# Optimization experiments

Hardware: AMD Instinct MI355X
Metric: run time of the kernel (lower is better)

The kernel has to match this reference:

```python
import jax, jax.numpy as jnp
import numpy as np

# norse default LIFParameters
DT = 1e-3
TAU_SYN_INV = 200.0
TAU_MEM_INV = 100.0
V_LEAK = 0.0
V_TH = 1.0
V_RESET = 0.0


def heaviside(x):
    return (x > 0).astype(x.dtype)


def setup_inputs() -> dict:
    key = jax.random.key(0)
    ks = jax.random.split(key, 5)
    T, B, I, H, O = 14, 4096, 2048, 1024, 128
    x = (jax.random.uniform(ks[0], (T, B, I), dtype=jnp.float32) < 0.2).astype(jnp.float32)  # spike train
    w_in = jax.random.normal(ks[1], (H, I), dtype=jnp.float32) * (1.0 / np.sqrt(I))
    w_rec = jax.random.normal(ks[2], (H, H), dtype=jnp.float32) * (1.0 / np.sqrt(H))
    out_w = jax.random.normal(ks[3], (O, H), dtype=jnp.float32) * (1.0 / np.sqrt(H))
    out_b = jax.random.normal(ks[4], (O,), dtype=jnp.float32) * 0.01
    return {"x": x, "w_in": w_in, "w_rec": w_rec, "out_w": out_w, "out_b": out_b}


def reference(x, w_in, w_rec, out_w, out_b):
    T, B, _ = x.shape
    H = w_in.shape[0]
    z0 = jnp.zeros((B, H), dtype=x.dtype)
    v0 = jnp.full((B, H), V_LEAK, dtype=x.dtype)
    i0 = jnp.zeros((B, H), dtype=x.dtype)

    def step(carry, x_t):
        z, v, i = carry
        v_dec = v + DT * TAU_MEM_INV * ((V_LEAK - v) + i)   # membrane integration
        i_dec = i - DT * TAU_SYN_INV * i                    # synaptic decay
        z_new = heaviside(v_dec - V_TH)                     # spike
        v_new = (1.0 - z_new) * v_dec + z_new * V_RESET     # reset
        i_new = i_dec + x_t @ w_in.T + z @ w_rec.T          # input + recurrent current
        return (z_new, v_new, i_new), None

    (z_T, _, _), _ = jax.lax.scan(step, (z0, v0, i0), x)
    return z_T @ out_w.T + out_b
```

## Files before the change

### kernel.cpp

```cpp
#include <hip/hip_runtime.h>
#include <stdint.h>

#define T_STEPS 14
#define B_DIM   4096
#define I_DIM   2048
#define H_DIM   1024
#define O_DIM   128
#define K_TOT   3072
#define ZBYTES  ((size_t)B_DIM * H_DIM)

#define WSCALE_F 33554432.0f

typedef __bf16  bf16x8  __attribute__((ext_vector_type(8)));
typedef float   floatx4 __attribute__((ext_vector_type(4)));
typedef int     int4v   __attribute__((ext_vector_type(4)));
typedef int     int16v  __attribute__((ext_vector_type(16)));
typedef unsigned long long u64;

__device__ __forceinline__ uint16_t f2bf_rne(float f) {
    uint32_t u = __float_as_uint(f);
    u += 0x7fffu + ((u >> 16) & 1u);
    return (uint16_t)(u >> 16);
}
__device__ __forceinline__ float bf2f(uint16_t h) {
    return __uint_as_float(((uint32_t)h) << 16);
}

__device__ __forceinline__ void gload_lds16(const void* g, void* l) {
    __builtin_amdgcn_global_load_lds((__attribute__((address_space(1))) void*)g,
                                     (__attribute__((address_space(3))) void*)l, 16, 0, 0);
}


__global__ void split_w_kernel(const float* __restrict__ w_in, const float* __restrict__ w_rec,
                               int8_t* __restrict__ WB) {
    int idx = blockIdx.x * 256 + threadIdx.x;
    int h = idx / K_TOT;
    int k = idx - h * K_TOT;
    float w = (k < I_DIM) ? w_in[(size_t)h * I_DIM + k]
                          : w_rec[(size_t)h * H_DIM + (k - I_DIM)];
    int W  = __float2int_rn(w * WSCALE_F);
    int d0 = (int8_t)(W & 0xFF);
    int r1 = (W - d0) >> 8;
    int d1 = (int8_t)(r1 & 0xFF);
    int d2 = (r1 - d1) >> 8;
    int nt = h >> 5, n32 = h & 31;
    int ktw = k >> 7, k128 = k & 127;
    int kk = k128 >> 5, half = (k128 >> 4) & 1, j = k128 & 15;
    int lane = half * 32 + n32;
    size_t base = (size_t)(nt * 24 + ktw) * 12288 + kk * 1024 + lane * 16 + j;
    WB[base] = (int8_t)d0; WB[base + 4096] = (int8_t)d1; WB[base + 8192] = (int8_t)d2;
}

__global__ void split_ow_kernel(const float* __restrict__ out_w, uint16_t* __restrict__ OW3) {
    int idx = blockIdx.x * 256 + threadIdx.x;
    float w = out_w[idx];
    uint16_t hi = f2bf_rne(w);
    float r1 = w - bf2f(hi);
    uint16_t mid = f2bf_rne(r1);
    float r2 = r1 - bf2f(mid);
    uint16_t lo = f2bf_rne(r2);
    const size_t S = (size_t)O_DIM * H_DIM;
    OW3[idx] = hi; OW3[idx + S] = mid; OW3[idx + 2 * S] = lo;
}

__global__ void cvt_x_kernel(const float* __restrict__ x, int8_t* __restrict__ xb) {
    size_t gid = (size_t)blockIdx.x * 256 + threadIdx.x;
    int g = (int)(gid & 1023);
    size_t chunk = gid >> 10;
    int kt   = (int)(chunk & 15);
    int mIdx = (int)((chunk >> 4) & 31);
    int t    = (int)(chunk >> 9);
    int group = g >> 8, kk = (g >> 6) & 3, lane = g & 63;
    int half = lane >> 5, row32 = lane & 31;
    int b = mIdx * 128 + group * 32 + row32;
    int k = kt * 128 + kk * 32 + half * 16;
    const float4* src = (const float4*)(x + ((size_t)t * B_DIM + b) * I_DIM + k);
    union { int8_t bytes[16]; int4v v; } u;
#pragma unroll
    for (int q = 0; q < 4; ++q) {
        float4 f = src[q];
        u.bytes[q * 4 + 0] = (int8_t)(f.x > 0.5f);
        u.bytes[q * 4 + 1] = (int8_t)(f.y > 0.5f);
        u.bytes[q * 4 + 2] = (int8_t)(f.z > 0.5f);
        u.bytes[q * 4 + 3] = (int8_t)(f.w > 0.5f);
    }
    ((int4v*)xb)[gid] = u.v;
}

__global__ void zero_cnt_kernel(uint32_t* __restrict__ cnt) {
    __hip_atomic_store(&cnt[blockIdx.x * 256 + threadIdx.x], 0u,
                       __ATOMIC_RELAXED, __HIP_MEMORY_SCOPE_AGENT);
}

__device__ __forceinline__ void loadA(const int8_t* __restrict__ aP, int4v (&a)[4]) {
    a[0] = *(const int4v*)(aP);
    a[1] = *(const int4v*)(aP + 1024);
    a[2] = *(const int4v*)(aP + 2048);
    a[3] = *(const int4v*)(aP + 3072);
}

__device__ __forceinline__ void stage_b0(const int8_t* __restrict__ bChunk0,
                                         int8_t* sB0, int wave, int lane) {
    gload_lds16(bChunk0 + (size_t)wave * 1024 + lane * 16,       sB0 + wave * 1024);
    gload_lds16(bChunk0 + (size_t)(4 + wave) * 1024 + lane * 16, sB0 + (4 + wave) * 1024);
    gload_lds16(bChunk0 + (size_t)(8 + wave) * 1024 + lane * 16, sB0 + (8 + wave) * 1024);
}

__device__ __forceinline__ void lif_iter(const int8_t* __restrict__ aPn,
                                         const int8_t* __restrict__ bPn,
                                         const int8_t* cur, int8_t* nxt,
                                         int4v (&aA)[4],
                                         int wave, int lane, bool stage_next,
                                         int16v (&acc)[3]) {
    if (stage_next) {
        gload_lds16(bPn + (size_t)wave * 1024 + lane * 16,       nxt + wave * 1024);
        gload_lds16(bPn + (size_t)(4 + wave) * 1024 + lane * 16, nxt + (4 + wave) * 1024);
        gload_lds16(bPn + (size_t)(8 + wave) * 1024 + lane * 16, nxt + (8 + wave) * 1024);
        __builtin_amdgcn_sched_barrier(0);
        asm volatile("s_waitcnt vmcnt(3)" ::: "memory");
    } else {
        asm volatile("s_waitcnt vmcnt(0)" ::: "memory");
    }
    __builtin_amdgcn_s_barrier();
    __builtin_amdgcn_sched_barrier(0);
    __builtin_amdgcn_s_setprio(1);
#pragma unroll
    for (int kk = 0; kk < 4; ++kk) {
#pragma unroll
        for (int s = 0; s < 3; ++s) {
            int4v bF = *(const int4v*)(cur + s * 4096 + kk * 1024 + lane * 16);
            acc[s] = __builtin_amdgcn_mfma_i32_32x32x32_i8(aA[kk], bF, acc[s], 0, 0, 0);
        }
    }
    __builtin_amdgcn_s_setprio(0);
    __builtin_amdgcn_sched_barrier(0);
    if (aPn) loadA(aPn, aA);
    asm volatile("s_waitcnt lgkmcnt(0)" ::: "memory");
    __builtin_amdgcn_s_barrier();
}

template<int NKT>
__device__ __forceinline__ void run_phase(const int8_t* __restrict__ aW,
                                          const int8_t* __restrict__ bC,
                                          int8_t* sB0, int8_t* sB1,
                                          int4v (&aA)[4],
                                          int wave, int lane, int16v (&acc)[3]) {
#pragma unroll 1
    for (int kt = 0; kt + 2 < NKT; kt += 2) {
        lif_iter(aW + (size_t)(kt + 1) * 16384, bC + (size_t)(kt + 1) * 12288,
                 sB0, sB1, aA, wave, lane, true, acc);
        lif_iter(aW + (size_t)(kt + 2) * 16384, bC + (size_t)(kt + 2) * 12288,
                 sB1, sB0, aA, wave, lane, true, acc);
    }
    lif_iter(aW + (size_t)(NKT - 1) * 16384, bC + (size_t)(NKT - 1) * 12288,
             sB0, sB1, aA, wave, lane, true, acc);
    lif_iter(nullptr, nullptr, sB1, sB0, aA, wave, lane, false, acc);
}

__launch_bounds__(256, 4)
__global__ void lif_persist_kernel(const int8_t* __restrict__ Xall,
                                   const int8_t* __restrict__ WB,
                                   int8_t* __restrict__ ZS,
                                   uint16_t* __restrict__ Zbf,
                                   uint32_t* __restrict__ cnt) {
    __shared__ int8_t sB0[12288];
    __shared__ int8_t sB1[12288];
    __shared__ int8_t sZ[4096];

    const int tid  = threadIdx.x;
    const int wave = tid >> 6, lane = tid & 63;
    const int lane32 = lane & 31, hl = lane >> 5;

    const int bid = blockIdx.x;
    const int xs = bid & 7, q = bid >> 3;
    const int mIdx = xs * 4 + (q & 3);
    const int nt   = q >> 2;

    const int mBase = mIdx * 128, nBase = nt * 32;
    const int8_t* wbStrip = WB + (size_t)nt * 24 * 12288;
    const int fragOff = wave * 4096 + lane * 16;

    float vmem[16], isyn[16];
#pragma unroll
    for (int r = 0; r < 16; ++r) { vmem[r] = 0.0f; isyn[r] = 0.0f; }

    int4v aA[4];

    stage_b0(wbStrip, sB0, wave, lane);
    loadA(Xall + (size_t)mIdx * 16 * 16384 + fragOff, aA);

    for (int t = 0; t < T_STEPS; ++t) {
        int16v acc[3] = {};

        const int8_t* XtW = Xall + (size_t)t * ((size_t)B_DIM * I_DIM)
                          + (size_t)mIdx * 16 * 16384 + fragOff;
        run_phase<16>(XtW, wbStrip, sB0, sB1, aA, wave, lane, acc);

        if (t > 0) {
            const int8_t* zbChunk = wbStrip + (size_t)16 * 12288;
            stage_b0(zbChunk, sB0, wave, lane);
            if (tid == 0) {
                const uint32_t* f = cnt + ((size_t)mIdx * 13 + (t - 1)) * 32;
                while (__hip_atomic_load((uint32_t*)f, __ATOMIC_RELAXED, __HIP_MEMORY_SCOPE_AGENT) < 32u)
                    __builtin_amdgcn_s_sleep(2);
            }
            __syncthreads();
            const int8_t* zW = ZS + (size_t)(t - 1) * ZBYTES + (size_t)mIdx * 8 * 16384 + fragOff;
            loadA(zW, aA);
            run_phase<8>(zW, zbChunk, sB0, sB1, aA, wave, lane, acc);
        }

        if (t + 1 < T_STEPS) {
            stage_b0(wbStrip, sB0, wave, lane);
            loadA(Xall + (size_t)(t + 1) * ((size_t)B_DIM * I_DIM)
                  + (size_t)mIdx * 16 * 16384 + fragOff, aA);
        }

#pragma unroll
        for (int r = 0; r < 16; ++r) {
#pragma clang fp contract(off)
            float cur = (float)acc[2][r] * (1.0f / 512.0f)
                      + (float)acc[1][r] * (1.0f / 131072.0f)
                      + (float)acc[0][r] * (1.0f / 33554432.0f);
            int row = (r & 3) + 8 * (r >> 2) + 4 * hl;
            float v_dec = vmem[r] + 0.1f * ((0.0f - vmem[r]) + isyn[r]);
            float i_dec = isyn[r] - 0.2f * isyn[r];
            bool z = (v_dec > 1.0f);
            vmem[r] = z ? 0.0f : v_dec;
            isyn[r] = i_dec + cur;
            if (t == T_STEPS - 1) {
                int b = mBase + wave * 32 + row;
                int h = nBase + lane32;
                Zbf[(size_t)b * H_DIM + h] = z ? (uint16_t)0x3F80 : (uint16_t)0;
            } else {
                sZ[wave * 1024 + ((lane32 >> 4) * 32 + row) * 16 + (lane32 & 15)]
                    = z ? (int8_t)1 : (int8_t)0;
            }
        }

        if (t < T_STEPS - 1) {
            __syncthreads();
            const u64* sp = (const u64*)&sZ[tid * 16];
            u64 v0 = sp[0], v1 = sp[1];
            int8_t* dst = ZS + (size_t)t * ZBYTES + ((size_t)mIdx * 8 + (nt >> 2)) * 16384
                        + (tid >> 6) * 4096 + (nt & 3) * 1024 + (tid & 63) * 16;
            __hip_atomic_store((u64*)dst,       v0, __ATOMIC_RELAXED, __HIP_MEMORY_SCOPE_AGENT);
            __hip_atomic_store((u64*)(dst + 8), v1, __ATOMIC_RELAXED, __HIP_MEMORY_SCOPE_AGENT);
            __syncthreads();
            if (tid == 0)
                __hip_atomic_fetch_add(&cnt[((size_t)mIdx * 13 + t) * 32], 1u,
                                       __ATOMIC_RELAXED, __HIP_MEMORY_SCOPE_AGENT);
        }
    }
}

__launch_bounds__(256)
__global__ void out_gemm_kernel(const uint16_t* __restrict__ Zfin,
                                const uint16_t* __restrict__ OW3,
                                const float* __restrict__ out_b,
                                float* __restrict__ out) {
    __shared__ uint16_t sA[16 * 32];
    __shared__ uint16_t sB[3][128 * 32];

    const int tid  = threadIdx.x;
    const int wave = tid >> 6, lane = tid & 63;
    const int quad = lane >> 4, col = lane & 15;

    const int mBase = blockIdx.x * 16;

    floatx4 acc[2] = {};

    const int ldRow = lane >> 2;
    const int ldCol = (lane & 3) * 8;

    for (int kt = 0; kt < H_DIM / 32; ++kt) {
        const int kb = kt * 32;
        __syncthreads();
        if (wave == 0) {
            const uint16_t* g = Zfin + (size_t)(mBase + ldRow) * H_DIM + kb + ldCol;
            gload_lds16(g, &sA[0]);
        }
#pragma unroll
        for (int s = 0; s < 3; ++s) {
            const uint16_t* wsrc = OW3 + (size_t)s * O_DIM * H_DIM;
#pragma unroll
            for (int j = 0; j < 2; ++j) {
                const int rseg = j * 4 + wave;
                const uint16_t* g = wsrc + (size_t)(rseg * 16 + ldRow) * H_DIM + kb + ldCol;
                gload_lds16(g, &sB[s][rseg * 16 * 32]);
            }
        }
        __syncthreads();

        bf16x8 aF = *reinterpret_cast<const bf16x8*>(&sA[col * 32 + quad * 8]);
#pragma unroll
        for (int s = 0; s < 3; ++s) {
#pragma unroll
            for (int ni = 0; ni < 2; ++ni) {
                int row = wave * 32 + ni * 16 + col;
                bf16x8 bF = *reinterpret_cast<const bf16x8*>(&sB[s][row * 32 + quad * 8]);
                acc[ni] = __builtin_amdgcn_mfma_f32_16x16x32_bf16(aF, bF, acc[ni], 0, 0, 0);
            }
        }
    }

    {
#pragma clang fp contract(off)
#pragma unroll
        for (int ni = 0; ni < 2; ++ni)
#pragma unroll
            for (int r = 0; r < 4; ++r) {
                int b = mBase + quad * 4 + r;
                int h = wave * 32 + ni * 16 + col;
                out[(size_t)b * O_DIM + h] = acc[ni][r] + out_b[h];
            }
    }
}

extern "C" void kernel_launch(void* const* d_in, const int* in_sizes, int n_in,
                              void* d_out, int out_size, void* d_ws, size_t ws_size,
                              hipStream_t stream) {
    const float* x     = (const float*)d_in[0];
    const float* w_in  = (const float*)d_in[1];
    const float* w_rec = (const float*)d_in[2];
    const float* out_w = (const float*)d_in[3];
    const float* out_b = (const float*)d_in[4];
    float* out = (float*)d_out;

    char* ws = (char*)d_ws;
    size_t off = 0;
    int8_t*   WB   = (int8_t*)(ws + off);   off += (size_t)3 * H_DIM * K_TOT;
    uint16_t* OW3  = (uint16_t*)(ws + off); off += (size_t)3 * O_DIM * H_DIM * 2;
    int8_t*   Xall = (int8_t*)(ws + off);   off += (size_t)T_STEPS * B_DIM * I_DIM;
    uint16_t* Zbf  = (uint16_t*)(ws + off); off += (size_t)B_DIM * H_DIM * 2;
    int8_t*   ZS   = (int8_t*)(ws + off);   off += (size_t)13 * ZBYTES;
    uint32_t* CNT  = (uint32_t*)(ws + off); off += (size_t)32 * 13 * 32 * 4;

    split_w_kernel<<<(H_DIM * K_TOT) / 256, 256, 0, stream>>>(w_in, w_rec, WB);
    split_ow_kernel<<<(O_DIM * H_DIM) / 256, 256, 0, stream>>>(out_w, OW3);
    cvt_x_kernel<<<(int)(((size_t)T_STEPS * B_DIM * I_DIM / 16) / 256), 256, 0, stream>>>(x, Xall);
    zero_cnt_kernel<<<(32 * 13 * 32) / 256, 256, 0, stream>>>(CNT);

    lif_persist_kernel<<<dim3(1024), dim3(256), 0, stream>>>(Xall, WB, ZS, Zbf, CNT);

    out_gemm_kernel<<<B_DIM / 16, 256, 0, stream>>>(Zbf, OW3, out_b, out);
}
```

Before: 1.295 ms.

## Widen persistent LIF tile to 64 hidden columns per block, halving grid

Each persistent block now computes two 32-column N tiles (64 hidden units) instead of one. It stages both weight strips into doubled LDS buffers and reuses each loaded A fragment (spikes) across six MFMAs instead of three. This roughly halves global/L2 reads of the activation operand and halves the grid to 512 blocks, with the per-step arrival count reduced to 16. In exchange, LDS and register use per block double and occupancy bounds drop to 2 blocks per CU, which reduces latency hiding and parallelism.

```diff
diff --git a/kernel.cpp b/kernel.cpp
--- a/kernel.cpp
+++ b/kernel.cpp
@@ -100,25 +100,28 @@
     a[3] = *(const int4v*)(aP + 3072);
 }
 
-__device__ __forceinline__ void stage_b0(const int8_t* __restrict__ bChunk0,
-                                         int8_t* sB0, int wave, int lane) {
-    gload_lds16(bChunk0 + (size_t)wave * 1024 + lane * 16,       sB0 + wave * 1024);
-    gload_lds16(bChunk0 + (size_t)(4 + wave) * 1024 + lane * 16, sB0 + (4 + wave) * 1024);
-    gload_lds16(bChunk0 + (size_t)(8 + wave) * 1024 + lane * 16, sB0 + (8 + wave) * 1024);
+__device__ __forceinline__ void stage_b(const int8_t* __restrict__ bA,
+                                        const int8_t* __restrict__ bB,
+                                        int8_t* dst, int wave, int lane) {
+    gload_lds16(bA + (size_t)wave * 1024 + lane * 16,       dst + wave * 1024);
+    gload_lds16(bA + (size_t)(4 + wave) * 1024 + lane * 16, dst + (4 + wave) * 1024);
+    gload_lds16(bA + (size_t)(8 + wave) * 1024 + lane * 16, dst + (8 + wave) * 1024);
+    gload_lds16(bB + (size_t)wave * 1024 + lane * 16,       dst + 12288 + wave * 1024);
+    gload_lds16(bB + (size_t)(4 + wave) * 1024 + lane * 16, dst + 12288 + (4 + wave) * 1024);
+    gload_lds16(bB + (size_t)(8 + wave) * 1024 + lane * 16, dst + 12288 + (8 + wave) * 1024);
 }
 
 __device__ __forceinline__ void lif_iter(const int8_t* __restrict__ aPn,
-                                         const int8_t* __restrict__ bPn,
+                                         const int8_t* __restrict__ bPnA,
+                                         const int8_t* __restrict__ bPnB,
                                          const int8_t* cur, int8_t* nxt,
                                          int4v (&aA)[4],
                                          int wave, int lane, bool stage_next,
-                                         int16v (&acc)[3]) {
+                                         int16v (&acc)[2][3]) {
     if (stage_next) {
-        gload_lds16(bPn + (size_t)wave * 1024 + lane * 16,       nxt + wave * 1024);
-        gload_lds16(bPn + (size_t)(4 + wave) * 1024 + lane * 16, nxt + (4 + wave) * 1024);
-        gload_lds16(bPn + (size_t)(8 + wave) * 1024 + lane * 16, nxt + (8 + wave) * 1024);
+        stage_b(bPnA, bPnB, nxt, wave, lane);
         __builtin_amdgcn_sched_barrier(0);
-        asm volatile("s_waitcnt vmcnt(3)" ::: "memory");
+        asm volatile("s_waitcnt vmcnt(6)" ::: "memory");
     } else {
         asm volatile("s_waitcnt vmcnt(0)" ::: "memory");
     }
@@ -128,9 +131,12 @@
 #pragma unroll
     for (int kk = 0; kk < 4; ++kk) {
 #pragma unroll
-        for (int s = 0; s < 3; ++s) {
-            int4v bF = *(const int4v*)(cur + s * 4096 + kk * 1024 + lane * 16);
-            acc[s] = __builtin_amdgcn_mfma_i32_32x32x32_i8(aA[kk], bF, acc[s], 0, 0, 0);
+        for (int n = 0; n < 2; ++n) {
+#pragma unroll
+            for (int s = 0; s < 3; ++s) {
+                int4v bF = *(const int4v*)(cur + n * 12288 + s * 4096 + kk * 1024 + lane * 16);
+                acc[n][s] = __builtin_amdgcn_mfma_i32_32x32x32_i8(aA[kk], bF, acc[n][s], 0, 0, 0);
+            }
         }
     }
     __builtin_amdgcn_s_setprio(0);
@@ -142,31 +148,32 @@
 
 template<int NKT>
 __device__ __forceinline__ void run_phase(const int8_t* __restrict__ aW,
-                                          const int8_t* __restrict__ bC,
+                                          const int8_t* __restrict__ bA,
+                                          const int8_t* __restrict__ bB,
                                           int8_t* sB0, int8_t* sB1,
                                           int4v (&aA)[4],
-                                          int wave, int lane, int16v (&acc)[3]) {
+                                          int wave, int lane, int16v (&acc)[2][3]) {
 #pragma unroll 1
     for (int kt = 0; kt + 2 < NKT; kt += 2) {
-        lif_iter(aW + (size_t)(kt + 1) * 16384, bC + (size_t)(kt + 1) * 12288,
-                 sB0, sB1, aA, wave, lane, true, acc);
-        lif_iter(aW + (size_t)(kt + 2) * 16384, bC + (size_t)(kt + 2) * 12288,
-                 sB1, sB0, aA, wave, lane, true, acc);
-    }
-    lif_iter(aW + (size_t)(NKT - 1) * 16384, bC + (size_t)(NKT - 1) * 12288,
-             sB0, sB1, aA, wave, lane, true, acc);
-    lif_iter(nullptr, nullptr, sB1, sB0, aA, wave, lane, false, acc);
-}
-
-__launch_bounds__(256, 4)
+        lif_iter(aW + (size_t)(kt + 1) * 16384, bA + (size_t)(kt + 1) * 12288,
+                 bB + (size_t)(kt + 1) * 12288, sB0, sB1, aA, wave, lane, true, acc);
+        lif_iter(aW + (size_t)(kt + 2) * 16384, bA + (size_t)(kt + 2) * 12288,
+                 bB + (size_t)(kt + 2) * 12288, sB1, sB0, aA, wave, lane, true, acc);
+    }
+    lif_iter(aW + (size_t)(NKT - 1) * 16384, bA + (size_t)(NKT - 1) * 12288,
+             bB + (size_t)(NKT - 1) * 12288, sB0, sB1, aA, wave, lane, true, acc);
+    lif_iter(nullptr, nullptr, nullptr, sB1, sB0, aA, wave, lane, false, acc);
+}
+
+__launch_bounds__(256, 2)
 __global__ void lif_persist_kernel(const int8_t* __restrict__ Xall,
                                    const int8_t* __restrict__ WB,
                                    int8_t* __restrict__ ZS,
                                    uint16_t* __restrict__ Zbf,
                                    uint32_t* __restrict__ cnt) {
-    __shared__ int8_t sB0[12288];
-    __shared__ int8_t sB1[12288];
-    __shared__ int8_t sZ[4096];
+    __shared__ int8_t sB0[24576];
+    __shared__ int8_t sB1[24576];
+    __shared__ int8_t sZ[8192];
 
     const int tid  = threadIdx.x;
     const int wave = tid >> 6, lane = tid & 63;
@@ -175,78 +182,89 @@
     const int bid = blockIdx.x;
     const int xs = bid & 7, q = bid >> 3;
     const int mIdx = xs * 4 + (q & 3);
-    const int nt   = q >> 2;
-
-    const int mBase = mIdx * 128, nBase = nt * 32;
-    const int8_t* wbStrip = WB + (size_t)nt * 24 * 12288;
+    const int nt2  = q >> 2;
+
+    const int mBase = mIdx * 128, nBase = nt2 * 64;
+    const int8_t* wbA = WB + (size_t)(2 * nt2) * 24 * 12288;
+    const int8_t* wbB = WB + (size_t)(2 * nt2 + 1) * 24 * 12288;
     const int fragOff = wave * 4096 + lane * 16;
 
-    float vmem[16], isyn[16];
-#pragma unroll
-    for (int r = 0; r < 16; ++r) { vmem[r] = 0.0f; isyn[r] = 0.0f; }
+    float vmem[2][16], isyn[2][16];
+#pragma unroll
+    for (int n = 0; n < 2; ++n)
+#pragma unroll
+        for (int r = 0; r < 16; ++r) { vmem[n][r] = 0.0f; isyn[n][r] = 0.0f; }
 
     int4v aA[4];
 
-    stage_b0(wbStrip, sB0, wave, lane);
+    stage_b(wbA, wbB, sB0, wave, lane);
     loadA(Xall + (size_t)mIdx * 16 * 16384 + fragOff, aA);
 
     for (int t = 0; t < T_STEPS; ++t) {
-        int16v acc[3] = {};
+        int16v acc[2][3] = {};
 
         const int8_t* XtW = Xall + (size_t)t * ((size_t)B_DIM * I_DIM)
                           + (size_t)mIdx * 16 * 16384 + fragOff;
-        run_phase<16>(XtW, wbStrip, sB0, sB1, aA, wave, lane, acc);
+        run_phase<16>(XtW, wbA, wbB, sB0, sB1, aA, wave, lane, acc);
 
         if (t > 0) {
-            const int8_t* zbChunk = wbStrip + (size_t)16 * 12288;
-            stage_b0(zbChunk, sB0, wave, lane);
+            const int8_t* zbA = wbA + (size_t)16 * 12288;
+            const int8_t* zbB = wbB + (size_t)16 * 12288;
+            stage_b(zbA, zbB, sB0, wave, lane);
             if (tid == 0) {
                 const uint32_t* f = cnt + ((size_t)mIdx * 13 + (t - 1)) * 32;
-                while (__hip_atomic_load((uint32_t*)f, __ATOMIC_RELAXED, __HIP_MEMORY_SCOPE_AGENT) < 32u)
+                while (__hip_atomic_load((uint32_t*)f, __ATOMIC_RELAXED, __HIP_MEMORY_SCOPE_AGENT) < 16u)
                     __builtin_amdgcn_s_sleep(2);
             }
             __syncthreads();
             const int8_t* zW = ZS + (size_t)(t - 1) * ZBYTES + (size_t)mIdx * 8 * 16384 + fragOff;
             loadA(zW, aA);
-            run_phase<8>(zW, zbChunk, sB0, sB1, aA, wave, lane, acc);
+            run_phase<8>(zW, zbA, zbB, sB0, sB1, aA, wave, lane, acc);
         }
 
         if (t + 1 < T_STEPS) {
-            stage_b0(wbStrip, sB0, wave, lane);
+            stage_b(wbA, wbB, sB0, wave, lane);
             loadA(Xall + (size_t)(t + 1) * ((size_t)B_DIM * I_DIM)
                   + (size_t)mIdx * 16 * 16384 + fragOff, aA);
         }
 
 #pragma unroll
-        for (int r = 0; r < 16; ++r) {
+        for (int n = 0; n < 2; ++n) {
+#pragma unroll
+            for (int r = 0; r < 16; ++r) {
 #pragma clang fp contract(off)
-            float cur = (float)acc[2][r] * (1.0f / 512.0f)
-                      + (float)acc[1][r] * (1.0f / 131072.0f)
-                      + (float)acc[0][r] * (1.0f / 33554432.0f);
-            int row = (r & 3) + 8 * (r >> 2) + 4 * hl;
-            float v_dec = vmem[r] + 0.1f * ((0.0f - vmem[r]) + isyn[r]);
-            float i_dec = isyn[r] - 0.2f * isyn[r];
-            bool z = (v_dec > 1.0f);
-            vmem[r] = z ? 0.0f : v_dec;
-            isyn[r] = i_dec + cur;
-            if (t == T_STEPS - 1) {
-                int b = mBase + wave * 32 + row;
-                int h = nBase + lane32;
-                Zbf[(size_t)b * H_DIM + h] = z ? (uint16_t)0x3F80 : (uint16_t)0;
-            } else {
-                sZ[wave * 1024 + ((lane32 >> 4) * 32 + row) * 16 + (lane32 & 15)]
-                    = z ? (int8_t)1 : (int8_t)0;
+                float cur = (float)acc[n][2][r] * (1.0f / 512.0f)
+                          + (float)acc[n][1][r] * (1.0f / 131072.0f)
+                          + (float)acc[n][0][r] * (1.0f / 33554432.0f);
+                int row = (r & 3) + 8 * (r >> 2) + 4 * hl;
+                float v_dec = vmem[n][r] + 0.1f * ((0.0f - vmem[n][r]) + isyn[n][r]);
+                float i_dec = isyn[n][r] - 0.2f * isyn[n][r];
+                bool z = (v_dec > 1.0f);
+                vmem[n][r] = z ? 0.0f : v_dec;
+                isyn[n][r] = i_dec + cur;
+                if (t == T_STEPS - 1) {
+                    int b = mBase + wave * 32 + row;
+                    int h = nBase + n * 32 + lane32;
+                    Zbf[(size_t)b * H_DIM + h] = z ? (uint16_t)0x3F80 : (uint16_t)0;
+                } else {
+                    sZ[n * 4096 + wave * 1024 + ((lane32 >> 4) * 32 + row) * 16 + (lane32 & 15)]
+                        = z ? (int8_t)1 : (int8_t)0;
+                }
             }
         }
 
         if (t < T_STEPS - 1) {
             __syncthreads();
-            const u64* sp = (const u64*)&sZ[tid * 16];
-            u64 v0 = sp[0], v1 = sp[1];
-            int8_t* dst = ZS + (size_t)t * ZBYTES + ((size_t)mIdx * 8 + (nt >> 2)) * 16384
-                        + (tid >> 6) * 4096 + (nt & 3) * 1024 + (tid & 63) * 16;
-            __hip_atomic_store((u64*)dst,       v0, __ATOMIC_RELAXED, __HIP_MEMORY_SCOPE_AGENT);
-            __hip_atomic_store((u64*)(dst + 8), v1, __ATOMIC_RELAXED, __HIP_MEMORY_SCOPE_AGENT);
+#pragma unroll
+            for (int n = 0; n < 2; ++n) {
+                const u64* sp = (const u64*)&sZ[n * 4096 + tid * 16];
+                u64 v0 = sp[0], v1 = sp[1];
+                const int ntn = nt2 * 2 + n;
+                int8_t* dst = ZS + (size_t)t * ZBYTES + ((size_t)mIdx * 8 + (ntn >> 2)) * 16384
+                            + (tid >> 6) * 4096 + (ntn & 3) * 1024 + (tid & 63) * 16;
+                __hip_atomic_store((u64*)dst,       v0, __ATOMIC_RELAXED, __HIP_MEMORY_SCOPE_AGENT);
+                __hip_atomic_store((u64*)(dst + 8), v1, __ATOMIC_RELAXED, __HIP_MEMORY_SCOPE_AGENT);
+            }
             __syncthreads();
             if (tid == 0)
                 __hip_atomic_fetch_add(&cnt[((size_t)mIdx * 13 + t) * 32], 1u,
@@ -342,7 +360,7 @@
     cvt_x_kernel<<<(int)(((size_t)T_STEPS * B_DIM * I_DIM / 16) / 256), 256, 0, stream>>>(x, Xall);
     zero_cnt_kernel<<<(32 * 13 * 32) / 256, 256, 0, stream>>>(CNT);
 
-    lif_persist_kernel<<<dim3(1024), dim3(256), 0, stream>>>(Xall, WB, ZS, Zbf, CNT);
+    lif_persist_kernel<<<dim3(512), dim3(256), 0, stream>>>(Xall, WB, ZS, Zbf, CNT);
 
     out_gemm_kernel<<<B_DIM / 16, 256, 0, stream>>>(Zbf, OW3, out_b, out);
 }
```

New measurement: 1.254 ms. 1.03x faster.
